# Performance work log

Hardware: AMD Instinct MI355X
Metric: run time of the kernel (lower is better)

## Reference

```python
import jax, jax.numpy as jnp
import numpy as np

P = 8      # input_path_dim
D = 64     # cde_state_dim
W = 16     # signature_window_size
OUT = 32   # output_path_dim
II, JJ = np.triu_indices(P, k=1)   # Lyndon words of length 2: (i, j) with i < j
L = P + II.shape[0]                # logsig size at depth 2 = 8 + 28 = 36


def lipswish(x):
    return 0.909 * jax.nn.silu(x)


def setup_inputs() -> dict:
    key = jax.random.key(0)
    ks = jax.random.split(key, 16)
    s = lambda *sh: 1.0 / np.sqrt(sh[-1])
    inp = {
        "control_values": jax.random.normal(ks[0], (32, 257, P), dtype=jnp.float32),
        # initial-condition MLP: P -> 128 -> 128 -> D, lipswish activations
        "ic_w1": jax.random.normal(ks[1], (128, P)) * s(128, P),
        "ic_b1": jnp.zeros((128,)),
        "ic_w2": jax.random.normal(ks[2], (128, 128)) * s(128, 128),
        "ic_b2": jnp.zeros((128,)),
        "ic_w3": jax.random.normal(ks[3], (D, 128)) * s(D, 128),
        "ic_b3": jnp.zeros((D,)),
        # vector-field MLP: D -> 128 -> 128 -> P*D, lipswish, final tanh
        "vf_w1": jax.random.normal(ks[4], (128, D)) * s(128, D),
        "vf_b1": jnp.zeros((128,)),
        "vf_w2": jax.random.normal(ks[5], (128, 128)) * s(128, 128),
        "vf_b2": jnp.zeros((128,)),
        "vf_w3": jax.random.normal(ks[6], (P * D, 128)) * s(P * D, 128),
        "vf_b3": jnp.zeros((P * D,)),
        # readout: D -> OUT
        "ro_w": jax.random.normal(ks[7], (OUT, D)) * s(OUT, D),
        "ro_b": jnp.zeros((OUT,)),
    }
    return {k: v.astype(jnp.float32) for k, v in inp.items()}


def _windowed_logsigs(x):
    """Depth-2 Lyndon log-signatures of piecewise-linear path x: (length, P) -> (n_windows, L)."""
    dx = jnp.diff(x, axis=0).reshape(-1, W, P)          # (nw, W, P) increments
    lev1 = dx.sum(axis=1)                               # (nw, P)
    pre = jnp.cumsum(dx, axis=1) - dx                   # X_k - X_0 within window
    s = jnp.einsum("wki,wkj->wij", pre, dx)             # iterated-integral cross terms
    area = 0.5 * (s - jnp.swapaxes(s, 1, 2))            # Levy area, antisymmetric
    lev2 = area[:, II, JJ]                              # Lyndon coords i<j: (nw, P*(P-1)/2)
    return jnp.concatenate([lev1, lev2], axis=1)        # (nw, L)


def reference(control_values, ic_w1, ic_b1, ic_w2, ic_b2, ic_w3, ic_b3,
              vf_w1, vf_b1, vf_w2, vf_b2, vf_w3, vf_b3, ro_w, ro_b):
    def ic_mlp(x):
        h = lipswish(ic_w1 @ x + ic_b1)
        h = lipswish(ic_w2 @ h + ic_b2)
        return ic_w3 @ h + ic_b3

    def vf(y):  # all P vector fields stacked: (P, D)
        h = lipswish(vf_w1 @ y + vf_b1)
        h = lipswish(vf_w2 @ h + vf_b2)
        return jnp.tanh(vf_w3 @ h + vf_b3).reshape(P, D)

    def vf_matrix(y):
        # Euclidean manifold: retract / project_to_tangent are identity.
        F = vf(y)                        # (P, D)  level-1 columns f_i(y)
        J = jax.jacfwd(vf)(y)            # (P, D, D) Jacobians df_a/dy
        M = jnp.einsum("ade,be->abd", J, F)     # M[a,b] = J_a @ f_b
        lev2 = M[JJ, II] - M[II, JJ]     # [f_i, f_j](y) = Jf_j f_i - Jf_i f_j
        return jnp.concatenate([F, lev2], axis=0).T  # (D, L)

    def solve_one(x):  # x: (length, P)
        logsigs = _windowed_logsigs(x)   # (nw, L)
        y0 = ic_mlp(x[0])
        def step(y, v):                  # one RK4 step per window (log-ODE)
            g = lambda z: vf_matrix(z) @ v
            k1 = g(y); k2 = g(y + 0.5 * k1); k3 = g(y + 0.5 * k2); k4 = g(y + k3)
            y2 = y + (k1 + 2.0 * k2 + 2.0 * k3 + k4) / 6.0
            return y2, y2
        _, ys = jax.lax.scan(step, y0, logsigs)
        hidden = jnp.concatenate([y0[None], ys], axis=0)   # (nw+1, D) evolving output
        return hidden @ ro_w.T + ro_b                      # readout, identity retract

    return jax.vmap(solve_one)(control_values)             # (B, nw+1, OUT)
```

## Files before the change

kernel.cpp:

```cpp
#include <hip/hip_runtime.h>
#include <math.h>

#define NT 1024

#define D_YCUR 0
#define D_KACC 64
#define D_T3   128
#define D_VSIG 640
#define D_HID  1216
#define D_X0   2304
#define D_TOTAL 2312

#define F_YB 0
#define F_H1 96
#define F_D1 256
#define F_H2 384
#define F_D2 544
#define F_FB 672
#define F_WM 1184
#define F_U1 1696
#define F_U2 2976
#define F_CM 4256
#define F_TOTAL 4320

static __device__ __forceinline__ double lipswish_d(double z, double* d) {
    double s = 1.0 / (1.0 + exp(-z));
    *d = 0.909 * s * (1.0 + z * (1.0 - s));
    return 0.909 * z * s;
}
static __device__ __forceinline__ float lipswish_f(float z, float* d) {
    float s = 1.0f / (1.0f + expf(-z));
    *d = 0.909f * s * (1.0f + z * (1.0f - s));
    return 0.909f * z * s;
}

template<int CTRL>
static __device__ __forceinline__ float dpp_mov_f(float v) {
    int xx = __builtin_amdgcn_update_dpp(0, __float_as_int(v), CTRL, 0xF, 0xF, false);
    return __int_as_float(xx);
}
static __device__ __forceinline__ float red8f(float v) {
    v += dpp_mov_f<0xB1>(v);
    v += dpp_mov_f<0x4E>(v);
    v += dpp_mov_f<0x141>(v);
    return v;
}
static __device__ __forceinline__ float red16f(float v) {
    v += dpp_mov_f<0xB1>(v);
    v += dpp_mov_f<0x4E>(v);
    v += dpp_mov_f<0x141>(v);
    v += dpp_mov_f<0x128>(v);
    return v;
}
static __device__ __forceinline__ float red4f(float v) {
    v += dpp_mov_f<0xB1>(v);
    v += dpp_mov_f<0x4E>(v);
    return v;
}
static __device__ __forceinline__ float red2f(float v) {
    return v + dpp_mov_f<0xB1>(v);
}

extern "C" __global__ void __launch_bounds__(NT, 1)
ncde_solve(const float* __restrict__ x,
           const float* __restrict__ ic_w1, const float* __restrict__ ic_b1,
           const float* __restrict__ ic_w2, const float* __restrict__ ic_b2,
           const float* __restrict__ ic_w3, const float* __restrict__ ic_b3,
           const float* __restrict__ vf_w1, const float* __restrict__ vf_b1,
           const float* __restrict__ vf_w2, const float* __restrict__ vf_b2,
           const float* __restrict__ vf_w3, const float* __restrict__ vf_b3,
           const float* __restrict__ ro_w,  const float* __restrict__ ro_b,
           float* __restrict__ out)
{
    __shared__ double smd[D_TOTAL];
    __shared__ __align__(16) float smf[F_TOTAL];

    const int t = threadIdx.x;
    const int b = blockIdx.x;
    const float* xb = x + (size_t)b * (257 * 8);

    const int o8 = t >> 3, p8 = t & 7;
    const int o16 = t >> 4, p16 = t & 15;
    const int m = t >> 2, q = t & 3;
    const int aT = t >> 7;

    float w1f[8];
    {
        const float4* s4 = reinterpret_cast<const float4*>(vf_w1 + o8 * 64 + 8 * p8);
        float4 v0 = s4[0], v1 = s4[1];
        w1f[0] = v0.x; w1f[1] = v0.y; w1f[2] = v0.z; w1f[3] = v0.w;
        w1f[4] = v1.x; w1f[5] = v1.y; w1f[6] = v1.z; w1f[7] = v1.w;
    }
    float w2f[16];
    {
        const float4* s4 = reinterpret_cast<const float4*>(vf_w2 + o8 * 128 + 16 * p8);
        #pragma unroll
        for (int jj = 0; jj < 4; ++jj) {
            float4 v = s4[jj];
            w2f[4 * jj] = v.x; w2f[4 * jj + 1] = v.y;
            w2f[4 * jj + 2] = v.z; w2f[4 * jj + 3] = v.w;
        }
    }
    float w1u[2][4];
    {
        float4 a = *reinterpret_cast<const float4*>(vf_w1 + o16 * 64 + 4 * p16);
        float4 c = *reinterpret_cast<const float4*>(vf_w1 + (o16 + 64) * 64 + 4 * p16);
        w1u[0][0] = a.x; w1u[0][1] = a.y; w1u[0][2] = a.z; w1u[0][3] = a.w;
        w1u[1][0] = c.x; w1u[1][1] = c.y; w1u[1][2] = c.z; w1u[1][3] = c.w;
    }
    float w2u[2][8];
    {
        const float4* sa = reinterpret_cast<const float4*>(vf_w2 + o16 * 128 + 8 * p16);
        const float4* sb = reinterpret_cast<const float4*>(vf_w2 + (o16 + 64) * 128 + 8 * p16);
        float4 a0 = sa[0], a1 = sa[1], c0 = sb[0], c1 = sb[1];
        w2u[0][0] = a0.x; w2u[0][1] = a0.y; w2u[0][2] = a0.z; w2u[0][3] = a0.w;
        w2u[0][4] = a1.x; w2u[0][5] = a1.y; w2u[0][6] = a1.z; w2u[0][7] = a1.w;
        w2u[1][0] = c0.x; w2u[1][1] = c0.y; w2u[1][2] = c0.z; w2u[1][3] = c0.w;
        w2u[1][4] = c1.x; w2u[1][5] = c1.y; w2u[1][6] = c1.z; w2u[1][7] = c1.w;
    }
    float w3a[32], w3b[32];
    {
        const float4* sa = reinterpret_cast<const float4*>(vf_w3 + (size_t)(2 * m) * 128 + 32 * q);
        const float4* sb = reinterpret_cast<const float4*>(vf_w3 + (size_t)(2 * m + 1) * 128 + 32 * q);
        #pragma unroll
        for (int jj = 0; jj < 8; ++jj) {
            float4 va = sa[jj], vb = sb[jj];
            w3a[4 * jj] = va.x; w3a[4 * jj + 1] = va.y; w3a[4 * jj + 2] = va.z; w3a[4 * jj + 3] = va.w;
            w3b[4 * jj] = vb.x; w3b[4 * jj + 1] = vb.y; w3b[4 * jj + 2] = vb.z; w3b[4 * jj + 3] = vb.w;
        }
    }
    const float b1o = vf_b1[o8];
    const float b2o = vf_b2[o8];
    const float b3a = vf_b3[2 * m];
    const float b3b = vf_b3[2 * m + 1];

    if (t < 8) smd[D_X0 + t] = (double)xb[t];
    if (t < 16) {
        const float* xr = xb + t * 16 * 8;
        double cum[8], area[28], prev[8];
        #pragma unroll
        for (int i = 0; i < 8; ++i) { cum[i] = 0.0; prev[i] = (double)xr[i]; }
        #pragma unroll
        for (int u = 0; u < 28; ++u) area[u] = 0.0;
        for (int k = 1; k <= 16; ++k) {
            double dx[8];
            #pragma unroll
            for (int i = 0; i < 8; ++i) {
                double c = (double)xr[k * 8 + i];
                dx[i] = c - prev[i];
                prev[i] = c;
            }
            #pragma unroll
            for (int i = 0; i < 7; ++i) {
                #pragma unroll
                for (int j = i + 1; j < 8; ++j) {
                    int u = 7 * i - (i * (i - 1)) / 2 + (j - i - 1);
                    area[u] += 0.5 * (cum[i] * dx[j] - cum[j] * dx[i]);
                }
            }
            #pragma unroll
            for (int i = 0; i < 8; ++i) cum[i] += dx[i];
        }
        #pragma unroll
        for (int i = 0; i < 8; ++i) smd[D_VSIG + t * 36 + i] = cum[i];
        #pragma unroll
        for (int u = 0; u < 28; ++u) smd[D_VSIG + t * 36 + 8 + u] = area[u];
    }
    __syncthreads();

    if (t < 128) {
        double acc = (double)ic_b1[t];
        #pragma unroll
        for (int e = 0; e < 8; ++e) acc += (double)ic_w1[t * 8 + e] * smd[D_X0 + e];
        double d;
        smd[D_T3 + t] = lipswish_d(acc, &d);
    }
    __syncthreads();
    if (t < 128) {
        const float4* wr = reinterpret_cast<const float4*>(ic_w2 + t * 128);
        double a0 = 0.0, a1 = 0.0, a2 = 0.0, a3 = 0.0;
        #pragma unroll
        for (int k = 0; k < 32; ++k) {
            float4 wv = wr[k];
            double2 h0 = *reinterpret_cast<const double2*>(&smd[D_T3 + 4 * k]);
            double2 h1 = *reinterpret_cast<const double2*>(&smd[D_T3 + 4 * k + 2]);
            a0 += (double)wv.x * h0.x; a1 += (double)wv.y * h0.y;
            a2 += (double)wv.z * h1.x; a3 += (double)wv.w * h1.y;
        }
        double d;
        smd[D_T3 + 128 + t] = lipswish_d((double)ic_b2[t] + (a0 + a2) + (a1 + a3), &d);
    }
    __syncthreads();
    if (t < 64) {
        const float4* wr = reinterpret_cast<const float4*>(ic_w3 + t * 128);
        double a0 = 0.0, a1 = 0.0, a2 = 0.0, a3 = 0.0;
        #pragma unroll
        for (int k = 0; k < 32; ++k) {
            float4 wv = wr[k];
            double2 h0 = *reinterpret_cast<const double2*>(&smd[D_T3 + 128 + 4 * k]);
            double2 h1 = *reinterpret_cast<const double2*>(&smd[D_T3 + 128 + 4 * k + 2]);
            a0 += (double)wv.x * h0.x; a1 += (double)wv.y * h0.y;
            a2 += (double)wv.z * h1.x; a3 += (double)wv.w * h1.y;
        }
        double y0 = (double)ic_b3[t] + (a0 + a2) + (a1 + a3);
        smd[D_YCUR + t] = y0;
        smd[D_HID + t]  = y0;
        smf[F_YB + t + 4 * (t >> 3)] = (float)y0;
        int a = t >> 3, bb = t & 7;
        double cv = 0.0;
        if (a != bb) {
            int i = a < bb ? a : bb;
            int j = a < bb ? bb : a;
            int pidx = 7 * i - (i * (i - 1)) / 2 + (j - i - 1);
            double vv = smd[D_VSIG + 8 + pidx];
            cv = (a > bb) ? vv : -vv;
        }
        smf[F_CM + t] = (float)cv;
    }
    __syncthreads();

    for (int w = 0; w < 16; ++w) {
        for (int stage = 0; stage < 4; ++stage) {
            {
                float4 y0 = *reinterpret_cast<const float4*>(&smf[F_YB + 12 * p8]);
                float4 y1 = *reinterpret_cast<const float4*>(&smf[F_YB + 12 * p8 + 4]);
                float acc = w1f[0] * y0.x + w1f[1] * y0.y + w1f[2] * y0.z + w1f[3] * y0.w
                          + w1f[4] * y1.x + w1f[5] * y1.y + w1f[6] * y1.z + w1f[7] * y1.w;
                acc = red8f(acc);
                if (p8 == 0) {
                    float d;
                    smf[F_H1 + o8 + 4 * (o8 >> 4)] = lipswish_f(acc + b1o, &d);
                    smf[F_D1 + o8] = d;
                }
            }
            __syncthreads();
            {
                const float4* hv = reinterpret_cast<const float4*>(&smf[F_H1 + 20 * p8]);
                float4 h0 = hv[0], h1 = hv[1], h2 = hv[2], h3 = hv[3];
                float a0 = w2f[0] * h0.x + w2f[1] * h0.y + w2f[2] * h0.z + w2f[3] * h0.w
                         + w2f[4] * h1.x + w2f[5] * h1.y + w2f[6] * h1.z + w2f[7] * h1.w;
                float a1 = w2f[8] * h2.x + w2f[9] * h2.y + w2f[10] * h2.z + w2f[11] * h2.w
                         + w2f[12] * h3.x + w2f[13] * h3.y + w2f[14] * h3.z + w2f[15] * h3.w;
                float acc = red8f(a0 + a1);
                if (p8 == 0) {
                    float d;
                    smf[F_H2 + o8 + 4 * (o8 >> 4)] = lipswish_f(acc + b2o, &d);
                    smf[F_D2 + o8] = d;
                }
            }
            __syncthreads();
            float F0 = 0.0f, F1 = 0.0f;
            {
                float a0 = 0.0f, a1 = 0.0f;
                #pragma unroll
                for (int jj = 0; jj < 8; ++jj) {
                    float4 hv = *reinterpret_cast<const float4*>(
                        &smf[F_H2 + 40 * q + 4 * jj + 4 * (jj >> 2)]);
                    a0 += w3a[4 * jj] * hv.x + w3a[4 * jj + 1] * hv.y
                        + w3a[4 * jj + 2] * hv.z + w3a[4 * jj + 3] * hv.w;
                    a1 += w3b[4 * jj] * hv.x + w3b[4 * jj + 1] * hv.y
                        + w3b[4 * jj + 2] * hv.z + w3b[4 * jj + 3] * hv.w;
                }
                a0 = red4f(a0);
                a1 = red4f(a1);
                if (q == 0) {
                    F0 = tanhf(a0 + b3a);
                    F1 = tanhf(a1 + b3b);
                    float2 fv; fv.x = F0; fv.y = F1;
                    *reinterpret_cast<float2*>(&smf[F_FB + 2 * m]) = fv;
                }
            }
            __syncthreads();
            {
                int kw = t & 1, ew = (t >> 1) & 63;
                float s = 0.0f;
                #pragma unroll
                for (int i = 0; i < 4; ++i) {
                    int bb = 4 * kw + i;
                    s += smf[F_CM + aT * 8 + bb] * smf[F_FB + bb * 64 + ew];
                }
                s = red2f(s);
                if (kw == 0) smf[F_WM + aT * 64 + ew] = s;
            }
            __syncthreads();
            {
                float d1a = smf[F_D1 + o16], d1b = smf[F_D1 + o16 + 64];
                int ob = F_U1 + o16 + 4 * (o16 >> 4);
                #pragma unroll
                for (int a = 0; a < 8; ++a) {
                    float4 mv = *reinterpret_cast<const float4*>(&smf[F_WM + a * 64 + 4 * p16]);
                    float a0 = w1u[0][0] * mv.x + w1u[0][1] * mv.y + w1u[0][2] * mv.z + w1u[0][3] * mv.w;
                    float a1 = w1u[1][0] * mv.x + w1u[1][1] * mv.y + w1u[1][2] * mv.z + w1u[1][3] * mv.w;
                    a0 = red16f(a0);
                    a1 = red16f(a1);
                    if (p16 == 0) {
                        smf[ob + a * 160]      = a0 * d1a;
                        smf[ob + a * 160 + 80] = a1 * d1b;
                    }
                }
            }
            __syncthreads();
            {
                float d2a = smf[F_D2 + o16], d2b = smf[F_D2 + o16 + 64];
                int ib = 8 * p16 + 4 * (p16 >> 1);
                int ob = F_U2 + o16 + 4 * (o16 >> 4);
                #pragma unroll
                for (int a = 0; a < 8; ++a) {
                    float4 u0 = *reinterpret_cast<const float4*>(&smf[F_U1 + a * 160 + ib]);
                    float4 u1 = *reinterpret_cast<const float4*>(&smf[F_U1 + a * 160 + ib + 4]);
                    float a0 = w2u[0][0] * u0.x + w2u[0][1] * u0.y + w2u[0][2] * u0.z + w2u[0][3] * u0.w
                             + w2u[0][4] * u1.x + w2u[0][5] * u1.y + w2u[0][6] * u1.z + w2u[0][7] * u1.w;
                    float a1 = w2u[1][0] * u0.x + w2u[1][1] * u0.y + w2u[1][2] * u0.z + w2u[1][3] * u0.w
                             + w2u[1][4] * u1.x + w2u[1][5] * u1.y + w2u[1][6] * u1.z + w2u[1][7] * u1.w;
                    a0 = red16f(a0);
                    a1 = red16f(a1);
                    if (p16 == 0) {
                        smf[ob + a * 160]      = a0 * d2a;
                        smf[ob + a * 160 + 80] = a1 * d2b;
                    }
                }
            }
            __syncthreads();
            {
                float a0 = 0.0f, a1 = 0.0f;
                #pragma unroll
                for (int jj = 0; jj < 8; ++jj) {
                    float4 uv = *reinterpret_cast<const float4*>(
                        &smf[F_U2 + aT * 160 + 40 * q + 4 * jj + 4 * (jj >> 2)]);
                    a0 += w3a[4 * jj] * uv.x + w3a[4 * jj + 1] * uv.y
                        + w3a[4 * jj + 2] * uv.z + w3a[4 * jj + 3] * uv.w;
                    a1 += w3b[4 * jj] * uv.x + w3b[4 * jj + 1] * uv.y
                        + w3b[4 * jj + 2] * uv.z + w3b[4 * jj + 3] * uv.w;
                }
                a0 = red4f(a0);
                a1 = red4f(a1);
                if (q == 0) {
                    double va = smd[D_VSIG + w * 36 + aT];
                    double2 tv;
                    tv.x = va * (double)F0 + (1.0 - (double)F0 * F0) * (double)a0;
                    tv.y = va * (double)F1 + (1.0 - (double)F1 * F1) * (double)a1;
                    *reinterpret_cast<double2*>(&smd[D_T3 + 2 * m]) = tv;
                }
            }
            __syncthreads();
            if (t < 64) {
                double g = 0.0;
                #pragma unroll
                for (int a = 0; a < 8; ++a) g += smd[D_T3 + a * 64 + t];
                double y = smd[D_YCUR + t];
                int yp = F_YB + t + 4 * (t >> 3);
                if (stage == 0)      { smd[D_KACC + t] = g;        smf[yp] = (float)(y + 0.5 * g); }
                else if (stage == 1) { smd[D_KACC + t] += 2.0 * g; smf[yp] = (float)(y + 0.5 * g); }
                else if (stage == 2) { smd[D_KACC + t] += 2.0 * g; smf[yp] = (float)(y + g); }
                else {
                    double yn = y + (smd[D_KACC + t] + g) * (1.0 / 6.0);
                    smd[D_YCUR + t] = yn;
                    smf[yp] = (float)yn;
                    smd[D_HID + (w + 1) * 64 + t] = yn;
                }
            } else if (t < 128 && stage == 3 && w < 15) {
                int idx = t - 64;
                int a = idx >> 3, bb = idx & 7;
                double cv = 0.0;
                if (a != bb) {
                    int i = a < bb ? a : bb;
                    int j = a < bb ? bb : a;
                    int pidx = 7 * i - (i * (i - 1)) / 2 + (j - i - 1);
                    double vv = smd[D_VSIG + (w + 1) * 36 + 8 + pidx];
                    cv = (a > bb) ? vv : -vv;
                }
                smf[F_CM + idx] = (float)cv;
            }
            __syncthreads();
        }
    }

    for (int idx = t; idx < 544; idx += NT) {
        int s = idx >> 5, oo = idx & 31;
        double acc = (double)ro_b[oo];
        const float* wr = ro_w + oo * 64;
        const double* hr = &smd[D_HID + s * 64];
        #pragma unroll
        for (int d = 0; d < 64; ++d) acc += (double)wr[d] * hr[d];
        out[(size_t)b * 544 + idx] = (float)acc;
    }
}

extern "C" void kernel_launch(void* const* d_in, const int* in_sizes, int n_in,
                              void* d_out, int out_size, void* d_ws, size_t ws_size,
                              hipStream_t stream) {
    const float* x     = (const float*)d_in[0];
    const float* ic_w1 = (const float*)d_in[1];
    const float* ic_b1 = (const float*)d_in[2];
    const float* ic_w2 = (const float*)d_in[3];
    const float* ic_b2 = (const float*)d_in[4];
    const float* ic_w3 = (const float*)d_in[5];
    const float* ic_b3 = (const float*)d_in[6];
    const float* vf_w1 = (const float*)d_in[7];
    const float* vf_b1 = (const float*)d_in[8];
    const float* vf_w2 = (const float*)d_in[9];
    const float* vf_b2 = (const float*)d_in[10];
    const float* vf_w3 = (const float*)d_in[11];
    const float* vf_b3 = (const float*)d_in[12];
    const float* ro_w  = (const float*)d_in[13];
    const float* ro_b  = (const float*)d_in[14];
    float* out = (float*)d_out;

    int B = in_sizes[0] / (257 * 8);
    hipLaunchKernelGGL(ncde_solve, dim3(B), dim3(NT), 0, stream,
                       x, ic_w1, ic_b1, ic_w2, ic_b2, ic_w3, ic_b3,
                       vf_w1, vf_b1, vf_w2, vf_b2, vf_w3, vf_b3, ro_w, ro_b, out);
}
```

Before: 639.4 us.

## Remap thread-to-output assignment so each lane computes four rows per reduction

Reassigns the work of every MLP and Jacobian-vector stage so that each thread group produces four output rows at once. Layers 1 and 2 now run on only the first 512 threads, and the 8 Lie-bracket directions are split across two halves of the block. The W3 matvec moves from 4-lane to 8-lane reductions with four rows per group. The aim is to reuse each shared-memory load across more FMAs and to cut the number of DPP reductions. The cost is more weights held in registers and idle threads during the early layers.

```diff
diff --git a/kernel.cpp b/kernel.cpp
--- a/kernel.cpp
+++ b/kernel.cpp
@@ -51,14 +51,6 @@
     v += dpp_mov_f<0x141>(v);
     v += dpp_mov_f<0x128>(v);
     return v;
-}
-static __device__ __forceinline__ float red4f(float v) {
-    v += dpp_mov_f<0xB1>(v);
-    v += dpp_mov_f<0x4E>(v);
-    return v;
-}
-static __device__ __forceinline__ float red2f(float v) {
-    return v + dpp_mov_f<0xB1>(v);
 }
 
 extern "C" __global__ void __launch_bounds__(NT, 1)
@@ -79,60 +71,45 @@
     const int b = blockIdx.x;
     const float* xb = x + (size_t)b * (257 * 8);
 
-    const int o8 = t >> 3, p8 = t & 7;
-    const int o16 = t >> 4, p16 = t & 15;
-    const int m = t >> 2, q = t & 3;
-    const int aT = t >> 7;
-
-    float w1f[8];
-    {
-        const float4* s4 = reinterpret_cast<const float4*>(vf_w1 + o8 * 64 + 8 * p8);
+    const int oq = (t >> 4) & 31;
+    const int p16 = t & 15;
+    const int dh = t >> 9;
+    const int mq = t >> 3;
+    const int p8 = t & 7;
+    const int aT = mq >> 4;
+
+    float w1u[4][4];
+    #pragma unroll
+    for (int r = 0; r < 4; ++r) {
+        float4 v = *reinterpret_cast<const float4*>(vf_w1 + (4 * oq + r) * 64 + 4 * p16);
+        w1u[r][0] = v.x; w1u[r][1] = v.y; w1u[r][2] = v.z; w1u[r][3] = v.w;
+    }
+    float w2u[4][8];
+    #pragma unroll
+    for (int r = 0; r < 4; ++r) {
+        const float4* s4 = reinterpret_cast<const float4*>(vf_w2 + (4 * oq + r) * 128 + 8 * p16);
         float4 v0 = s4[0], v1 = s4[1];
-        w1f[0] = v0.x; w1f[1] = v0.y; w1f[2] = v0.z; w1f[3] = v0.w;
-        w1f[4] = v1.x; w1f[5] = v1.y; w1f[6] = v1.z; w1f[7] = v1.w;
-    }
-    float w2f[16];
-    {
-        const float4* s4 = reinterpret_cast<const float4*>(vf_w2 + o8 * 128 + 16 * p8);
+        w2u[r][0] = v0.x; w2u[r][1] = v0.y; w2u[r][2] = v0.z; w2u[r][3] = v0.w;
+        w2u[r][4] = v1.x; w2u[r][5] = v1.y; w2u[r][6] = v1.z; w2u[r][7] = v1.w;
+    }
+    float w3q[4][16];
+    #pragma unroll
+    for (int r = 0; r < 4; ++r) {
+        const float4* s4 = reinterpret_cast<const float4*>(vf_w3 + (size_t)(4 * mq + r) * 128 + 16 * p8);
         #pragma unroll
         for (int jj = 0; jj < 4; ++jj) {
             float4 v = s4[jj];
-            w2f[4 * jj] = v.x; w2f[4 * jj + 1] = v.y;
-            w2f[4 * jj + 2] = v.z; w2f[4 * jj + 3] = v.w;
-        }
-    }
-    float w1u[2][4];
-    {
-        float4 a = *reinterpret_cast<const float4*>(vf_w1 + o16 * 64 + 4 * p16);
-        float4 c = *reinterpret_cast<const float4*>(vf_w1 + (o16 + 64) * 64 + 4 * p16);
-        w1u[0][0] = a.x; w1u[0][1] = a.y; w1u[0][2] = a.z; w1u[0][3] = a.w;
-        w1u[1][0] = c.x; w1u[1][1] = c.y; w1u[1][2] = c.z; w1u[1][3] = c.w;
-    }
-    float w2u[2][8];
-    {
-        const float4* sa = reinterpret_cast<const float4*>(vf_w2 + o16 * 128 + 8 * p16);
-        const float4* sb = reinterpret_cast<const float4*>(vf_w2 + (o16 + 64) * 128 + 8 * p16);
-        float4 a0 = sa[0], a1 = sa[1], c0 = sb[0], c1 = sb[1];
-        w2u[0][0] = a0.x; w2u[0][1] = a0.y; w2u[0][2] = a0.z; w2u[0][3] = a0.w;
-        w2u[0][4] = a1.x; w2u[0][5] = a1.y; w2u[0][6] = a1.z; w2u[0][7] = a1.w;
-        w2u[1][0] = c0.x; w2u[1][1] = c0.y; w2u[1][2] = c0.z; w2u[1][3] = c0.w;
-        w2u[1][4] = c1.x; w2u[1][5] = c1.y; w2u[1][6] = c1.z; w2u[1][7] = c1.w;
-    }
-    float w3a[32], w3b[32];
-    {
-        const float4* sa = reinterpret_cast<const float4*>(vf_w3 + (size_t)(2 * m) * 128 + 32 * q);
-        const float4* sb = reinterpret_cast<const float4*>(vf_w3 + (size_t)(2 * m + 1) * 128 + 32 * q);
-        #pragma unroll
-        for (int jj = 0; jj < 8; ++jj) {
-            float4 va = sa[jj], vb = sb[jj];
-            w3a[4 * jj] = va.x; w3a[4 * jj + 1] = va.y; w3a[4 * jj + 2] = va.z; w3a[4 * jj + 3] = va.w;
-            w3b[4 * jj] = vb.x; w3b[4 * jj + 1] = vb.y; w3b[4 * jj + 2] = vb.z; w3b[4 * jj + 3] = vb.w;
-        }
-    }
-    const float b1o = vf_b1[o8];
-    const float b2o = vf_b2[o8];
-    const float b3a = vf_b3[2 * m];
-    const float b3b = vf_b3[2 * m + 1];
+            w3q[r][4 * jj] = v.x; w3q[r][4 * jj + 1] = v.y;
+            w3q[r][4 * jj + 2] = v.z; w3q[r][4 * jj + 3] = v.w;
+        }
+    }
+    float b1q[4], b2q[4], b3q[4];
+    #pragma unroll
+    for (int r = 0; r < 4; ++r) {
+        b1q[r] = vf_b1[4 * oq + r];
+        b2q[r] = vf_b2[4 * oq + r];
+        b3q[r] = vf_b3[4 * mq + r];
+    }
 
     if (t < 8) smd[D_X0 + t] = (double)xb[t];
     if (t < 16) {
@@ -221,125 +198,152 @@
 
     for (int w = 0; w < 16; ++w) {
         for (int stage = 0; stage < 4; ++stage) {
+            if (dh == 0) {
+                float4 yv = *reinterpret_cast<const float4*>(&smf[F_YB + 4 * p16 + 4 * (p16 >> 1)]);
+                float acc0 = w1u[0][0] * yv.x + w1u[0][1] * yv.y + w1u[0][2] * yv.z + w1u[0][3] * yv.w;
+                float acc1 = w1u[1][0] * yv.x + w1u[1][1] * yv.y + w1u[1][2] * yv.z + w1u[1][3] * yv.w;
+                float acc2 = w1u[2][0] * yv.x + w1u[2][1] * yv.y + w1u[2][2] * yv.z + w1u[2][3] * yv.w;
+                float acc3 = w1u[3][0] * yv.x + w1u[3][1] * yv.y + w1u[3][2] * yv.z + w1u[3][3] * yv.w;
+                acc0 = red16f(acc0); acc1 = red16f(acc1);
+                acc2 = red16f(acc2); acc3 = red16f(acc3);
+                if (p16 == 0) {
+                    float4 hv, dv;
+                    hv.x = lipswish_f(acc0 + b1q[0], &dv.x);
+                    hv.y = lipswish_f(acc1 + b1q[1], &dv.y);
+                    hv.z = lipswish_f(acc2 + b1q[2], &dv.z);
+                    hv.w = lipswish_f(acc3 + b1q[3], &dv.w);
+                    *reinterpret_cast<float4*>(&smf[F_H1 + 4 * oq + 4 * (oq >> 2)]) = hv;
+                    *reinterpret_cast<float4*>(&smf[F_D1 + 4 * oq]) = dv;
+                }
+            }
+            __syncthreads();
+            if (dh == 0) {
+                int hb = 8 * p16 + 4 * (p16 >> 1);
+                float4 h0 = *reinterpret_cast<const float4*>(&smf[F_H1 + hb]);
+                float4 h1 = *reinterpret_cast<const float4*>(&smf[F_H1 + hb + 4]);
+                float acc[4];
+                #pragma unroll
+                for (int r = 0; r < 4; ++r) {
+                    acc[r] = w2u[r][0] * h0.x + w2u[r][1] * h0.y + w2u[r][2] * h0.z + w2u[r][3] * h0.w
+                           + w2u[r][4] * h1.x + w2u[r][5] * h1.y + w2u[r][6] * h1.z + w2u[r][7] * h1.w;
+                    acc[r] = red16f(acc[r]);
+                }
+                if (p16 == 0) {
+                    float4 hv, dv;
+                    hv.x = lipswish_f(acc[0] + b2q[0], &dv.x);
+                    hv.y = lipswish_f(acc[1] + b2q[1], &dv.y);
+                    hv.z = lipswish_f(acc[2] + b2q[2], &dv.z);
+                    hv.w = lipswish_f(acc[3] + b2q[3], &dv.w);
+                    *reinterpret_cast<float4*>(&smf[F_H2 + 4 * oq + 4 * (oq >> 2)]) = hv;
+                    *reinterpret_cast<float4*>(&smf[F_D2 + 4 * oq]) = dv;
+                }
+            }
+            __syncthreads();
+            float Fq[4] = {0.0f, 0.0f, 0.0f, 0.0f};
             {
-                float4 y0 = *reinterpret_cast<const float4*>(&smf[F_YB + 12 * p8]);
-                float4 y1 = *reinterpret_cast<const float4*>(&smf[F_YB + 12 * p8 + 4]);
-                float acc = w1f[0] * y0.x + w1f[1] * y0.y + w1f[2] * y0.z + w1f[3] * y0.w
-                          + w1f[4] * y1.x + w1f[5] * y1.y + w1f[6] * y1.z + w1f[7] * y1.w;
-                acc = red8f(acc);
+                float acc[4] = {0.0f, 0.0f, 0.0f, 0.0f};
+                #pragma unroll
+                for (int k = 0; k < 4; ++k) {
+                    float4 hv = *reinterpret_cast<const float4*>(&smf[F_H2 + 20 * p8 + 4 * k]);
+                    #pragma unroll
+                    for (int r = 0; r < 4; ++r)
+                        acc[r] += w3q[r][4 * k] * hv.x + w3q[r][4 * k + 1] * hv.y
+                                + w3q[r][4 * k + 2] * hv.z + w3q[r][4 * k + 3] * hv.w;
+                }
+                #pragma unroll
+                for (int r = 0; r < 4; ++r) acc[r] = red8f(acc[r]);
                 if (p8 == 0) {
-                    float d;
-                    smf[F_H1 + o8 + 4 * (o8 >> 4)] = lipswish_f(acc + b1o, &d);
-                    smf[F_D1 + o8] = d;
-                }
+                    float4 fv;
+                    Fq[0] = fv.x = tanhf(acc[0] + b3q[0]);
+                    Fq[1] = fv.y = tanhf(acc[1] + b3q[1]);
+                    Fq[2] = fv.z = tanhf(acc[2] + b3q[2]);
+                    Fq[3] = fv.w = tanhf(acc[3] + b3q[3]);
+                    *reinterpret_cast<float4*>(&smf[F_FB + 4 * mq]) = fv;
+                }
+            }
+            __syncthreads();
+            if (t < 128) {
+                int a = t >> 4, eq = t & 15;
+                float cm[8];
+                #pragma unroll
+                for (int bb = 0; bb < 8; ++bb) cm[bb] = smf[F_CM + a * 8 + bb];
+                float4 s; s.x = 0.0f; s.y = 0.0f; s.z = 0.0f; s.w = 0.0f;
+                #pragma unroll
+                for (int bb = 0; bb < 8; ++bb) {
+                    float4 fv = *reinterpret_cast<const float4*>(&smf[F_FB + bb * 64 + 4 * eq]);
+                    s.x += cm[bb] * fv.x; s.y += cm[bb] * fv.y;
+                    s.z += cm[bb] * fv.z; s.w += cm[bb] * fv.w;
+                }
+                *reinterpret_cast<float4*>(&smf[F_WM + a * 64 + 4 * eq]) = s;
             }
             __syncthreads();
             {
-                const float4* hv = reinterpret_cast<const float4*>(&smf[F_H1 + 20 * p8]);
-                float4 h0 = hv[0], h1 = hv[1], h2 = hv[2], h3 = hv[3];
-                float a0 = w2f[0] * h0.x + w2f[1] * h0.y + w2f[2] * h0.z + w2f[3] * h0.w
-                         + w2f[4] * h1.x + w2f[5] * h1.y + w2f[6] * h1.z + w2f[7] * h1.w;
-                float a1 = w2f[8] * h2.x + w2f[9] * h2.y + w2f[10] * h2.z + w2f[11] * h2.w
-                         + w2f[12] * h3.x + w2f[13] * h3.y + w2f[14] * h3.z + w2f[15] * h3.w;
-                float acc = red8f(a0 + a1);
-                if (p8 == 0) {
-                    float d;
-                    smf[F_H2 + o8 + 4 * (o8 >> 4)] = lipswish_f(acc + b2o, &d);
-                    smf[F_D2 + o8] = d;
-                }
-            }
-            __syncthreads();
-            float F0 = 0.0f, F1 = 0.0f;
+                #pragma unroll
+                for (int ai = 0; ai < 4; ++ai) {
+                    int a = 4 * dh + ai;
+                    float4 mv = *reinterpret_cast<const float4*>(&smf[F_WM + a * 64 + 4 * p16]);
+                    float acc[4];
+                    #pragma unroll
+                    for (int r = 0; r < 4; ++r) {
+                        acc[r] = w1u[r][0] * mv.x + w1u[r][1] * mv.y
+                               + w1u[r][2] * mv.z + w1u[r][3] * mv.w;
+                        acc[r] = red16f(acc[r]);
+                    }
+                    if (p16 == 0) {
+                        float4 dv = *reinterpret_cast<const float4*>(&smf[F_D1 + 4 * oq]);
+                        float4 uv;
+                        uv.x = acc[0] * dv.x; uv.y = acc[1] * dv.y;
+                        uv.z = acc[2] * dv.z; uv.w = acc[3] * dv.w;
+                        *reinterpret_cast<float4*>(&smf[F_U1 + a * 160 + 4 * oq + 4 * (oq >> 2)]) = uv;
+                    }
+                }
+            }
+            __syncthreads();
             {
-                float a0 = 0.0f, a1 = 0.0f;
-                #pragma unroll
-                for (int jj = 0; jj < 8; ++jj) {
-                    float4 hv = *reinterpret_cast<const float4*>(
-                        &smf[F_H2 + 40 * q + 4 * jj + 4 * (jj >> 2)]);
-                    a0 += w3a[4 * jj] * hv.x + w3a[4 * jj + 1] * hv.y
-                        + w3a[4 * jj + 2] * hv.z + w3a[4 * jj + 3] * hv.w;
-                    a1 += w3b[4 * jj] * hv.x + w3b[4 * jj + 1] * hv.y
-                        + w3b[4 * jj + 2] * hv.z + w3b[4 * jj + 3] * hv.w;
-                }
-                a0 = red4f(a0);
-                a1 = red4f(a1);
-                if (q == 0) {
-                    F0 = tanhf(a0 + b3a);
-                    F1 = tanhf(a1 + b3b);
-                    float2 fv; fv.x = F0; fv.y = F1;
-                    *reinterpret_cast<float2*>(&smf[F_FB + 2 * m]) = fv;
-                }
-            }
-            __syncthreads();
-            {
-                int kw = t & 1, ew = (t >> 1) & 63;
-                float s = 0.0f;
-                #pragma unroll
-                for (int i = 0; i < 4; ++i) {
-                    int bb = 4 * kw + i;
-                    s += smf[F_CM + aT * 8 + bb] * smf[F_FB + bb * 64 + ew];
-                }
-                s = red2f(s);
-                if (kw == 0) smf[F_WM + aT * 64 + ew] = s;
-            }
-            __syncthreads();
-            {
-                float d1a = smf[F_D1 + o16], d1b = smf[F_D1 + o16 + 64];
-                int ob = F_U1 + o16 + 4 * (o16 >> 4);
-                #pragma unroll
-                for (int a = 0; a < 8; ++a) {
-                    float4 mv = *reinterpret_cast<const float4*>(&smf[F_WM + a * 64 + 4 * p16]);
-                    float a0 = w1u[0][0] * mv.x + w1u[0][1] * mv.y + w1u[0][2] * mv.z + w1u[0][3] * mv.w;
-                    float a1 = w1u[1][0] * mv.x + w1u[1][1] * mv.y + w1u[1][2] * mv.z + w1u[1][3] * mv.w;
-                    a0 = red16f(a0);
-                    a1 = red16f(a1);
-                    if (p16 == 0) {
-                        smf[ob + a * 160]      = a0 * d1a;
-                        smf[ob + a * 160 + 80] = a1 * d1b;
-                    }
-                }
-            }
-            __syncthreads();
-            {
-                float d2a = smf[F_D2 + o16], d2b = smf[F_D2 + o16 + 64];
                 int ib = 8 * p16 + 4 * (p16 >> 1);
-                int ob = F_U2 + o16 + 4 * (o16 >> 4);
-                #pragma unroll
-                for (int a = 0; a < 8; ++a) {
+                #pragma unroll
+                for (int ai = 0; ai < 4; ++ai) {
+                    int a = 4 * dh + ai;
                     float4 u0 = *reinterpret_cast<const float4*>(&smf[F_U1 + a * 160 + ib]);
                     float4 u1 = *reinterpret_cast<const float4*>(&smf[F_U1 + a * 160 + ib + 4]);
-                    float a0 = w2u[0][0] * u0.x + w2u[0][1] * u0.y + w2u[0][2] * u0.z + w2u[0][3] * u0.w
-                             + w2u[0][4] * u1.x + w2u[0][5] * u1.y + w2u[0][6] * u1.z + w2u[0][7] * u1.w;
-                    float a1 = w2u[1][0] * u0.x + w2u[1][1] * u0.y + w2u[1][2] * u0.z + w2u[1][3] * u0.w
-                             + w2u[1][4] * u1.x + w2u[1][5] * u1.y + w2u[1][6] * u1.z + w2u[1][7] * u1.w;
-                    a0 = red16f(a0);
-                    a1 = red16f(a1);
+                    float acc[4];
+                    #pragma unroll
+                    for (int r = 0; r < 4; ++r) {
+                        acc[r] = w2u[r][0] * u0.x + w2u[r][1] * u0.y + w2u[r][2] * u0.z + w2u[r][3] * u0.w
+                               + w2u[r][4] * u1.x + w2u[r][5] * u1.y + w2u[r][6] * u1.z + w2u[r][7] * u1.w;
+                        acc[r] = red16f(acc[r]);
+                    }
                     if (p16 == 0) {
-                        smf[ob + a * 160]      = a0 * d2a;
-                        smf[ob + a * 160 + 80] = a1 * d2b;
+                        float4 dv = *reinterpret_cast<const float4*>(&smf[F_D2 + 4 * oq]);
+                        float4 uv;
+                        uv.x = acc[0] * dv.x; uv.y = acc[1] * dv.y;
+                        uv.z = acc[2] * dv.z; uv.w = acc[3] * dv.w;
+                        *reinterpret_cast<float4*>(&smf[F_U2 + a * 160 + 4 * oq + 4 * (oq >> 2)]) = uv;
                     }
                 }
             }
             __syncthreads();
             {
-                float a0 = 0.0f, a1 = 0.0f;
-                #pragma unroll
-                for (int jj = 0; jj < 8; ++jj) {
-                    float4 uv = *reinterpret_cast<const float4*>(
-                        &smf[F_U2 + aT * 160 + 40 * q + 4 * jj + 4 * (jj >> 2)]);
-                    a0 += w3a[4 * jj] * uv.x + w3a[4 * jj + 1] * uv.y
-                        + w3a[4 * jj + 2] * uv.z + w3a[4 * jj + 3] * uv.w;
-                    a1 += w3b[4 * jj] * uv.x + w3b[4 * jj + 1] * uv.y
-                        + w3b[4 * jj + 2] * uv.z + w3b[4 * jj + 3] * uv.w;
-                }
-                a0 = red4f(a0);
-                a1 = red4f(a1);
-                if (q == 0) {
+                float acc[4] = {0.0f, 0.0f, 0.0f, 0.0f};
+                #pragma unroll
+                for (int k = 0; k < 4; ++k) {
+                    float4 uv = *reinterpret_cast<const float4*>(&smf[F_U2 + aT * 160 + 20 * p8 + 4 * k]);
+                    #pragma unroll
+                    for (int r = 0; r < 4; ++r)
+                        acc[r] += w3q[r][4 * k] * uv.x + w3q[r][4 * k + 1] * uv.y
+                                + w3q[r][4 * k + 2] * uv.z + w3q[r][4 * k + 3] * uv.w;
+                }
+                #pragma unroll
+                for (int r = 0; r < 4; ++r) acc[r] = red8f(acc[r]);
+                if (p8 == 0) {
                     double va = smd[D_VSIG + w * 36 + aT];
-                    double2 tv;
-                    tv.x = va * (double)F0 + (1.0 - (double)F0 * F0) * (double)a0;
-                    tv.y = va * (double)F1 + (1.0 - (double)F1 * F1) * (double)a1;
-                    *reinterpret_cast<double2*>(&smd[D_T3 + 2 * m]) = tv;
+                    double2 t0, t1;
+                    t0.x = va * (double)Fq[0] + (1.0 - (double)Fq[0] * Fq[0]) * (double)acc[0];
+                    t0.y = va * (double)Fq[1] + (1.0 - (double)Fq[1] * Fq[1]) * (double)acc[1];
+                    t1.x = va * (double)Fq[2] + (1.0 - (double)Fq[2] * Fq[2]) * (double)acc[2];
+                    t1.y = va * (double)Fq[3] + (1.0 - (double)Fq[3] * Fq[3]) * (double)acc[3];
+                    *reinterpret_cast<double2*>(&smd[D_T3 + 4 * mq])     = t0;
+                    *reinterpret_cast<double2*>(&smd[D_T3 + 4 * mq + 2]) = t1;
                 }
             }
             __syncthreads();
```

After: 1.383 ms. 2.16x slower.
